# Kernel optimization log

Hardware: AMD Instinct MI355X
Metric: run time of the kernel (lower is better)

## Reference

```python
import jax, jax.numpy as jnp
import numpy as np

N_E, N_R, E = 100000, 1000, 1000000
E_HID, R_HID = 128, 128
NEG_SLOPE = 0.01


def _seg_softmax(logits, seg, num_segments):
    # torch_geometric.utils.softmax: per-segment max-subtracted softmax, +1e-16 in denom
    m = jax.ops.segment_max(logits, seg, num_segments=num_segments)
    m = jnp.where(jnp.isfinite(m), m, 0.0)  # empty segments
    z = jnp.exp(logits - m[seg])
    s = jax.ops.segment_sum(z, seg, num_segments=num_segments)
    return z / (s[seg] + 1e-16)


def setup_inputs() -> dict:
    key = jax.random.key(0)
    ks = jax.random.split(key, 10)
    s_e = 1.0 / np.sqrt(E_HID)
    s_r = 1.0 / np.sqrt(R_HID)
    s_2r = 1.0 / np.sqrt(2 * R_HID)
    return {
        "x_e": jax.random.normal(ks[0], (N_E, E_HID), jnp.float32),
        "x_r": jax.random.normal(ks[1], (N_R, R_HID), jnp.float32),
        "edge_index": jax.random.randint(ks[2], (2, E), 0, N_E, jnp.int32),
        "rel": jax.random.randint(ks[3], (E,), 0, N_R, jnp.int32),
        "rel_all": jax.random.randint(ks[4], (N_R,), 0, N_R, jnp.int32),
        "w_ah": jax.random.uniform(ks[5], (E_HID,), jnp.float32, -s_e, s_e),
        "w_at": jax.random.uniform(ks[6], (E_HID,), jnp.float32, -s_e, s_e),
        "w_ar": jax.random.uniform(ks[7], (R_HID,), jnp.float32, -s_r, s_r),
        "W_r1": jax.random.uniform(ks[8], (R_HID, 2 * R_HID), jnp.float32, -s_r, s_r),
        "b_r1": jnp.zeros((2 * R_HID,), jnp.float32),
        "W_r2": jax.random.uniform(ks[9], (2 * R_HID, R_HID), jnp.float32, -s_2r, s_2r),
        "b_r2": jnp.zeros((R_HID,), jnp.float32),
        "W_r": jax.random.uniform(jax.random.fold_in(key, 99), (2 * R_HID, 2 * R_HID), jnp.float32, -s_2r, s_2r),
        "b_r": jnp.zeros((2 * R_HID,), jnp.float32),
    }


def reference(x_e, x_r, edge_index, rel, rel_all, w_ah, w_at, w_ar,
              W_r1, b_r1, W_r2, b_r2, W_r, b_r):
    h, t = edge_index[0], edge_index[1]
    n_e = x_e.shape[0]

    # per-node/per-rel attention scores, gathered per edge
    e_h = (x_e @ w_ah)[h]          # [E]
    e_t = (x_e @ w_at)[t]          # [E]
    e_r = (x_r @ w_ar)[rel]        # [E]

    alpha_h = _seg_softmax(jax.nn.leaky_relu(e_h + e_r, NEG_SLOPE), h, n_e)
    alpha_t = _seg_softmax(jax.nn.leaky_relu(e_t + e_r, NEG_SLOPE), t, n_e)

    # relation transform (no activation in original)
    x_r2 = (x_r @ W_r1 + b_r1) @ W_r2 + b_r2   # [N_r, r_hidden]
    msg = x_r + x_r2                            # [N_r, r_hidden]

    # sparse.mm(adj, msg) == weighted scatter-add over edges
    msg_e = msg[rel]                            # [E, r_hidden]
    x_e_h = jax.ops.segment_sum(alpha_h[:, None] * msg_e, h, num_segments=n_e)
    x_e_t = jax.ops.segment_sum(alpha_t[:, None] * msg_e, t, num_segments=n_e)

    x = jnp.concatenate([x_e_h, x_e_t], axis=1)  # [N_e, 2*r_hidden]
    return x @ W_r + b_r
```

## Files before the change

kernel.cpp:

```cpp
#include <hip/hip_runtime.h>
#include <hip/hip_fp16.h>


#define CH1    2048
#define SUPW   4096
#define CAP1   45056
#define CH2    4096
#define CHUNK2 (CAP1 / CH2)
#define CAP2   1024
#define MAXD   64

__global__ __launch_bounds__(256) void k_scores(
    const float* __restrict__ xe, const float* __restrict__ xr,
    const float* __restrict__ wah, const float* __restrict__ wat, const float* __restrict__ war,
    float* __restrict__ eh, float* __restrict__ et, float* __restrict__ er,
    int nE, int nR) {
    int wid = (blockIdx.x * blockDim.x + threadIdx.x) >> 6;
    int lane = threadIdx.x & 63;
    if (wid < nE) {
        float2 x2 = *(const float2*)(xe + (size_t)wid * 128 + lane * 2);
        float2 a2 = *(const float2*)(wah + lane * 2);
        float2 b2 = *(const float2*)(wat + lane * 2);
        float dh = x2.x * a2.x + x2.y * a2.y;
        float dt = x2.x * b2.x + x2.y * b2.y;
        #pragma unroll
        for (int m = 32; m >= 1; m >>= 1) { dh += __shfl_xor(dh, m); dt += __shfl_xor(dt, m); }
        if (lane == 0) { eh[wid] = dh; et[wid] = dt; }
    } else if (wid < nE + nR) {
        int r = wid - nE;
        float2 x2 = *(const float2*)(xr + (size_t)r * 128 + lane * 2);
        float2 c2 = *(const float2*)(war + lane * 2);
        float d = x2.x * c2.x + x2.y * c2.y;
        #pragma unroll
        for (int m = 32; m >= 1; m >>= 1) d += __shfl_xor(d, m);
        if (lane == 0) er[r] = d;
    }
}

__global__ __launch_bounds__(256) void k_rel(
    const float* __restrict__ xr,
    const float* __restrict__ W1, const float* __restrict__ b1,
    const float* __restrict__ W2, const float* __restrict__ b2,
    const float* __restrict__ Wr,
    __half* __restrict__ Mh, __half* __restrict__ Mt) {
    __shared__ float xs[128];
    __shared__ float hs[256];
    __shared__ float ms[128];
    int r = blockIdx.x, j = threadIdx.x;
    if (j < 128) xs[j] = xr[(size_t)r * 128 + j];
    __syncthreads();
    {
        float acc = b1[j];
        #pragma unroll 4
        for (int k = 0; k < 128; ++k) acc += xs[k] * W1[k * 256 + j];
        hs[j] = acc;
    }
    __syncthreads();
    if (j < 128) {
        float acc = b2[j] + xs[j];
        #pragma unroll 4
        for (int k = 0; k < 256; ++k) acc += hs[k] * W2[k * 128 + j];
        ms[j] = acc;
    }
    __syncthreads();
    {
        float ah = 0.f, at_ = 0.f;
        #pragma unroll 4
        for (int i = 0; i < 128; ++i) {
            float m = ms[i];
            ah  += m * Wr[i * 256 + j];
            at_ += m * Wr[(128 + i) * 256 + j];
        }
        Mh[(size_t)r * 256 + j] = __float2half(ah);
        Mt[(size_t)r * 256 + j] = __float2half(at_);
    }
}

__global__ __launch_bounds__(256) void k_hist1(
    const int* __restrict__ ei, int* __restrict__ hist, int E) {
    __shared__ int cnt[64];
    int tid = threadIdx.x;
    if (tid < 64) cnt[tid] = 0;
    __syncthreads();
    int base = blockIdx.x * CH1;
    #pragma unroll
    for (int k = 0; k < CH1 / 256; ++k) {
        int e = base + k * 256 + tid;
        if (e < E) {
            unsigned vh = ((unsigned)ei[e]) << 1;
            unsigned vt = (((unsigned)ei[E + e]) << 1) | 1u;
            atomicAdd(&cnt[vh >> 12], 1);
            atomicAdd(&cnt[vt >> 12], 1);
        }
    }
    __syncthreads();
    if (tid < 64) hist[tid * 512 + blockIdx.x] = cnt[tid];
}

__global__ __launch_bounds__(256) void k_scanp(
    int* __restrict__ hist, int* __restrict__ bcur1,
    int* __restrict__ bcur2, int nbuck, int nblk) {
    __shared__ int wtot[4];
    int bin = blockIdx.x, tid = threadIdx.x, lane = tid & 63, wid = tid >> 6;
    int g = bin * 256 + tid;
    if (g < nbuck) bcur2[g] = 0;
    int j0 = 2 * tid, j1 = 2 * tid + 1;
    int v0 = (j0 < nblk) ? hist[bin * 512 + j0] : 0;
    int v1 = (j1 < nblk) ? hist[bin * 512 + j1] : 0;
    int ts = v0 + v1;
    int incl = ts;
    #pragma unroll
    for (int d = 1; d < 64; d <<= 1) { int u = __shfl_up(incl, d); if (lane >= d) incl += u; }
    if (lane == 63) wtot[wid] = incl;
    __syncthreads();
    int wbase = 0;
    for (int w = 0; w < wid; ++w) wbase += wtot[w];
    int excl = wbase + incl - ts;
    hist[bin * 512 + j0] = excl;
    hist[bin * 512 + j1] = excl + v0;
    if (tid == 255) bcur1[bin] = wbase + incl;
}

__global__ __launch_bounds__(256) void k_part1(
    const int* __restrict__ ei, const int* __restrict__ rel,
    const int* __restrict__ hist, unsigned* __restrict__ part1, int E) {
    __shared__ unsigned stage[CH1 * 2];
    __shared__ int cnt[64], offs_[64], cur[64], gb[64];
    int tid = threadIdx.x;
    if (tid < 64) cnt[tid] = 0;
    __syncthreads();
    int base = blockIdx.x * CH1;
    unsigned wh[CH1 / 256], wt[CH1 / 256];
    bool ve[CH1 / 256];
    #pragma unroll
    for (int k = 0; k < CH1 / 256; ++k) {
        int e = base + k * 256 + tid;
        ve[k] = (e < E);
        unsigned h = 0, t = 0, r = 0;
        if (ve[k]) { h = (unsigned)ei[e]; t = (unsigned)ei[E + e]; r = (unsigned)rel[e]; }
        unsigned vh = h << 1, vt = (t << 1) | 1u;
        wh[k] = ((vh >> 12) << 26) | ((vh & 4095u) << 10) | r;
        wt[k] = ((vt >> 12) << 26) | ((vt & 4095u) << 10) | r;
        if (ve[k]) { atomicAdd(&cnt[wh[k] >> 26], 1); atomicAdd(&cnt[wt[k] >> 26], 1); }
    }
    __syncthreads();
    if (tid < 64) {
        int v = cnt[tid], incl = v;
        #pragma unroll
        for (int d = 1; d < 64; d <<= 1) { int u = __shfl_up(incl, d); if (tid >= d) incl += u; }
        offs_[tid] = incl - v;
        cur[tid] = incl - v;
        gb[tid] = hist[tid * 512 + blockIdx.x];
    }
    __syncthreads();
    #pragma unroll
    for (int k = 0; k < CH1 / 256; ++k) {
        if (ve[k]) {
            int p = atomicAdd(&cur[wh[k] >> 26], 1); stage[p] = wh[k];
            int q = atomicAdd(&cur[wt[k] >> 26], 1); stage[q] = wt[k];
        }
    }
    __syncthreads();
    int total = offs_[63] + cnt[63];
    for (int p = tid; p < total; p += 256) {
        unsigned w = stage[p];
        int bin = w >> 26;
        int dst = gb[bin] + (p - offs_[bin]);
        if (dst < CAP1) part1[(size_t)bin * CAP1 + dst] = w & 0x03FFFFFFu;
    }
}

__global__ __launch_bounds__(256) void k_part2(
    const int* __restrict__ bcur1, const unsigned* __restrict__ part1,
    int* __restrict__ bcur2, unsigned short* __restrict__ part2) {
    int s = blockIdx.x / CHUNK2, c = blockIdx.x % CHUNK2;
    int cnt_s = min(bcur1[s], CAP1);
    int start = c * CH2;
    if (start >= cnt_s) return;
    __shared__ unsigned stage[CH2];
    __shared__ int cnt[64], offs_[64], cur[64], gb[64];
    int tid = threadIdx.x;
    if (tid < 64) cnt[tid] = 0;
    __syncthreads();
    unsigned w_[CH2 / 256];
    bool v_[CH2 / 256];
    #pragma unroll
    for (int k = 0; k < CH2 / 256; ++k) {
        int i = start + k * 256 + tid;
        v_[k] = (i < cnt_s);
        unsigned it = v_[k] ? part1[(size_t)s * CAP1 + i] : 0u;
        unsigned sb = (it >> 16) & 63u;
        unsigned entry = (((it >> 10) & 63u) << 10) | (it & 1023u);
        w_[k] = (sb << 16) | entry;
        if (v_[k]) atomicAdd(&cnt[sb], 1);
    }
    __syncthreads();
    if (tid < 64) {
        int v = cnt[tid], incl = v;
        #pragma unroll
        for (int d = 1; d < 64; d <<= 1) { int u = __shfl_up(incl, d); if (tid >= d) incl += u; }
        offs_[tid] = incl - v;
        cur[tid] = incl - v;
        gb[tid] = atomicAdd(&bcur2[s * 64 + tid], v);
    }
    __syncthreads();
    #pragma unroll
    for (int k = 0; k < CH2 / 256; ++k)
        if (v_[k]) { int p = atomicAdd(&cur[w_[k] >> 16], 1); stage[p] = w_[k]; }
    __syncthreads();
    int total = offs_[63] + cnt[63];
    for (int p = tid; p < total; p += 256) {
        unsigned w = stage[p];
        int sb = w >> 16;
        int dst = gb[sb] + (p - offs_[sb]);
        if (dst < CAP2) part2[((size_t)s * 64 + sb) * CAP2 + dst] = (unsigned short)w;
    }
}

__global__ __launch_bounds__(256) void k_group_out6(
    const int* __restrict__ bcur2, const unsigned short* __restrict__ part2,
    const float* __restrict__ eh, const float* __restrict__ et, const float* __restrict__ er,
    const __half* __restrict__ Mh, const __half* __restrict__ Mt,
    const float* __restrict__ br, float* __restrict__ out, int nE, int nR) {
    __shared__ unsigned short csr[CAP2];
    __shared__ float er_s[1024];
    __shared__ int cnt[64], offs_[64], cur[64];
    int b = blockIdx.x, tid = threadIdx.x;
    int count = min(bcur2[b], CAP2);
    if (tid < 64) cnt[tid] = 0;
    for (int i = tid; i < nR; i += 256) er_s[i] = er[i];
    __syncthreads();
    unsigned short ev[CAP2 / 256];
    bool val[CAP2 / 256];
    #pragma unroll
    for (int k = 0; k < CAP2 / 256; ++k) {
        int i = tid + k * 256;
        val[k] = (i < count);
        ev[k] = val[k] ? part2[(size_t)b * CAP2 + i] : (unsigned short)0;
        if (val[k]) atomicAdd(&cnt[ev[k] >> 10], 1);
    }
    __syncthreads();
    if (tid < 64) {
        int v = cnt[tid], incl = v;
        #pragma unroll
        for (int d = 1; d < 64; d <<= 1) { int u = __shfl_up(incl, d); if (tid >= d) incl += u; }
        offs_[tid] = incl - v;
        cur[tid] = incl - v;
    }
    __syncthreads();
    #pragma unroll
    for (int k = 0; k < CAP2 / 256; ++k) {
        if (val[k]) {
            int p = atomicAdd(&cur[ev[k] >> 10], 1);
            csr[p] = (unsigned short)(ev[k] & 1023u);
        }
    }
    __syncthreads();
    int lane = tid & 63, wid = tid >> 6;
    int half = lane >> 5, l31 = lane & 31;
    float4 bv = *(const float4*)(br + l31 * 8 + half * 4);
    int nbase = b * 32;
    for (int li = wid; li < 32; li += 4) {
        int n = nbase + li;
        if (n >= nE) break;
        int oH = offs_[2 * li];
        int oT = offs_[2 * li + 1];
        int dH = min(cur[2 * li] - oH, MAXD);
        int dT = min(cur[2 * li + 1] - oT, MAXD);
        float ehn = eh[n], etn = et[n];
        unsigned eHv = 0u, eTv = 0u;
        if (lane < dH) {
            int r = csr[oH + lane];
            float l = ehn + er_s[r]; l = l > 0.f ? l : 0.01f * l;
            eHv = (__float_as_uint(__expf(l)) & 0xFFFFFC00u) | (unsigned)r;
        }
        if (lane < dT) {
            int r = csr[oT + lane];
            float l = etn + er_s[r]; l = l > 0.f ? l : 0.01f * l;
            eTv = (__float_as_uint(__expf(l)) & 0xFFFFFC00u) | (unsigned)r;
        }
        float aH[8] = {0, 0, 0, 0, 0, 0, 0, 0};
        float aT[8] = {0, 0, 0, 0, 0, 0, 0, 0};
        float sH = 0.f, sT = 0.f;
        for (int j = 0; j < dH; j += 2) {
            unsigned c = (unsigned)__shfl((int)eHv, j + half);
            float z = __uint_as_float(c & 0xFFFFFC00u);
            uint4 m = *(const uint4*)(Mh + (((size_t)(c & 0x3FFu)) << 8) + (l31 << 3));
            const __half* hp = (const __half*)&m;
            #pragma unroll
            for (int q = 0; q < 8; ++q)
                aH[q] = fmaf(__half2float(hp[q]), z, aH[q]);
            sH += z;
        }
        for (int j = 0; j < dT; j += 2) {
            unsigned c = (unsigned)__shfl((int)eTv, j + half);
            float z = __uint_as_float(c & 0xFFFFFC00u);
            uint4 m = *(const uint4*)(Mt + (((size_t)(c & 0x3FFu)) << 8) + (l31 << 3));
            const __half* hp = (const __half*)&m;
            #pragma unroll
            for (int q = 0; q < 8; ++q)
                aT[q] = fmaf(__half2float(hp[q]), z, aT[q]);
            sT += z;
        }
        sH += __shfl_xor(sH, 32);
        sT += __shfl_xor(sT, 32);
        float hc[4], tc[4];
        #pragma unroll
        for (int q = 0; q < 4; ++q) {
            float sendH = half ? aH[q] : aH[4 + q];
            float mineH = half ? aH[4 + q] : aH[q];
            hc[q] = mineH + __shfl_xor(sendH, 32);
            float sendT = half ? aT[q] : aT[4 + q];
            float mineT = half ? aT[4 + q] : aT[q];
            tc[q] = mineT + __shfl_xor(sendT, 32);
        }
        float iH = 1.f / (sH + 1e-16f);
        float iT = 1.f / (sT + 1e-16f);
        float4 o;
        o.x = hc[0] * iH + tc[0] * iT + bv.x;
        o.y = hc[1] * iH + tc[1] * iT + bv.y;
        o.z = hc[2] * iH + tc[2] * iT + bv.z;
        o.w = hc[3] * iH + tc[3] * iT + bv.w;
        *(float4*)(out + (size_t)n * 256 + l31 * 8 + half * 4) = o;
    }
}

__global__ __launch_bounds__(256) void k_hist(
    const int* __restrict__ ei, int* __restrict__ deg, int E, int nE) {
    int e = blockIdx.x * blockDim.x + threadIdx.x;
    if (e >= E) return;
    atomicAdd(&deg[ei[e]], 1);
    atomicAdd(&deg[nE + ei[E + e]], 1);
}

__global__ __launch_bounds__(256) void k_scan1(
    const int* __restrict__ deg, int* __restrict__ offs, int* __restrict__ bsum, int N) {
    __shared__ int wtot[4];
    int tid = threadIdx.x, lane = tid & 63, wid = tid >> 6;
    int base = blockIdx.x * 1024 + tid * 4;
    int v[4];
    #pragma unroll
    for (int i = 0; i < 4; ++i) v[i] = (base + i < N) ? deg[base + i] : 0;
    int ts = v[0] + v[1] + v[2] + v[3];
    int incl = ts;
    #pragma unroll
    for (int d = 1; d < 64; d <<= 1) { int u = __shfl_up(incl, d); if (lane >= d) incl += u; }
    if (lane == 63) wtot[wid] = incl;
    __syncthreads();
    int wbase = 0;
    for (int w = 0; w < wid; ++w) wbase += wtot[w];
    int run = wbase + incl - ts;
    #pragma unroll
    for (int i = 0; i < 4; ++i) { if (base + i < N) offs[base + i] = run; run += v[i]; }
    if (tid == 255) bsum[blockIdx.x] = wbase + incl;
}

__global__ __launch_bounds__(256) void k_scan2(int* __restrict__ bsum, int NB) {
    __shared__ int wtot[4];
    int tid = threadIdx.x, lane = tid & 63, wid = tid >> 6;
    int v = (tid < NB) ? bsum[tid] : 0;
    int incl = v;
    #pragma unroll
    for (int d = 1; d < 64; d <<= 1) { int u = __shfl_up(incl, d); if (lane >= d) incl += u; }
    if (lane == 63) wtot[wid] = incl;
    __syncthreads();
    int wbase = 0;
    for (int w = 0; w < wid; ++w) wbase += wtot[w];
    if (tid < NB) bsum[tid] = wbase + incl - v;
}

__global__ __launch_bounds__(256) void k_scan3(
    int* __restrict__ offs, const int* __restrict__ bsum, int* __restrict__ cursor, int N) {
    int i = blockIdx.x * blockDim.x + threadIdx.x;
    if (i >= N) return;
    int v = offs[i] + bsum[i >> 10];
    offs[i] = v;
    cursor[i] = v;
}

__global__ __launch_bounds__(256) void k_scatter_offs(
    const int* __restrict__ ei, const int* __restrict__ rel,
    const float* __restrict__ eh, const float* __restrict__ et, const float* __restrict__ er,
    int* __restrict__ cursor, unsigned* __restrict__ csr, int E, int nE) {
    int e = blockIdx.x * blockDim.x + threadIdx.x;
    if (e >= E) return;
    int h = ei[e], t = ei[E + e], r = rel[e];
    float erv = er[r];
    float lh = eh[h] + erv; lh = lh > 0.f ? lh : 0.01f * lh;
    float lt = et[t] + erv; lt = lt > 0.f ? lt : 0.01f * lt;
    unsigned zh = (__float_as_uint(__expf(lh)) & 0xFFFFFC00u) | (unsigned)r;
    unsigned zt = (__float_as_uint(__expf(lt)) & 0xFFFFFC00u) | (unsigned)r;
    int ph = atomicAdd(&cursor[h], 1);
    csr[ph] = zh;
    int pt = atomicAdd(&cursor[nE + t], 1);
    csr[pt] = zt;
}

__global__ __launch_bounds__(256) void k_out_offs(
    const int* __restrict__ offs, const int* __restrict__ deg, const unsigned* __restrict__ csr,
    const __half* __restrict__ Mh, const __half* __restrict__ Mt, const float* __restrict__ br,
    float* __restrict__ out, int nE) {
    int wid = (blockIdx.x * blockDim.x + threadIdx.x) >> 6;
    int lane = threadIdx.x & 63;
    if (wid >= nE) return;
    int dH = deg[wid], dT = deg[nE + wid];
    size_t offH = (size_t)offs[wid], offT = (size_t)offs[nE + wid];
    float4 accH = {0, 0, 0, 0}, accT = {0, 0, 0, 0};
    float sH = 0.f, sT = 0.f;
    int dM = max(dH, dT);
    for (int b = 0; b < dM; b += 64) {
        int kH = min(64, dH - b);
        int kT = min(64, dT - b);
        unsigned eH = 0, eT = 0;
        if (lane < kH) eH = csr[offH + b + lane];
        if (lane < kT) eT = csr[offT + b + lane];
        int kk = max(kH, kT);
        for (int j = 0; j < kk; ++j) {
            unsigned cH = (unsigned)__shfl((int)eH, j);
            unsigned cT = (unsigned)__shfl((int)eT, j);
            if (j < kH) {
                float z = __uint_as_float(cH & 0xFFFFFC00u);
                int r = (int)(cH & 0x3FFu);
                const __half2* mp = (const __half2*)(Mh + ((size_t)r << 8) + (lane << 2));
                float2 m01 = __half22float2(mp[0]);
                float2 m23 = __half22float2(mp[1]);
                accH.x += z * m01.x; accH.y += z * m01.y;
                accH.z += z * m23.x; accH.w += z * m23.y;
                sH += z;
            }
            if (j < kT) {
                float z = __uint_as_float(cT & 0xFFFFFC00u);
                int r = (int)(cT & 0x3FFu);
                const __half2* mp = (const __half2*)(Mt + ((size_t)r << 8) + (lane << 2));
                float2 m01 = __half22float2(mp[0]);
                float2 m23 = __half22float2(mp[1]);
                accT.x += z * m01.x; accT.y += z * m01.y;
                accT.z += z * m23.x; accT.w += z * m23.y;
                sT += z;
            }
        }
    }
    float iH = 1.f / (sH + 1e-16f);
    float iT = 1.f / (sT + 1e-16f);
    float4 bv = *(const float4*)(br + lane * 4);
    float4 o;
    o.x = accH.x * iH + accT.x * iT + bv.x;
    o.y = accH.y * iH + accT.y * iT + bv.y;
    o.z = accH.z * iH + accT.z * iT + bv.z;
    o.w = accH.w * iH + accT.w * iT + bv.w;
    *(float4*)(out + (size_t)wid * 256 + lane * 4) = o;
}

extern "C" void kernel_launch(void* const* d_in, const int* in_sizes, int n_in,
                              void* d_out, int out_size, void* d_ws, size_t ws_size,
                              hipStream_t stream) {
    const float* xe  = (const float*)d_in[0];
    const float* xr  = (const float*)d_in[1];
    const int*   ei  = (const int*)d_in[2];
    const int*   rel = (const int*)d_in[3];
    const float* wah = (const float*)d_in[5];
    const float* wat = (const float*)d_in[6];
    const float* war = (const float*)d_in[7];
    const float* W1  = (const float*)d_in[8];
    const float* b1  = (const float*)d_in[9];
    const float* W2  = (const float*)d_in[10];
    const float* b2  = (const float*)d_in[11];
    const float* Wr  = (const float*)d_in[12];
    const float* br  = (const float*)d_in[13];
    float* out = (float*)d_out;

    const int nE = in_sizes[0] / 128;
    const int nR = in_sizes[1] / 128;
    const int E  = in_sizes[3];
    const int N  = 2 * nE;
    const int NSUP  = (N + SUPW - 1) / SUPW;
    const int NBUCK = NSUP * 64;
    const int NBLK1 = (E + CH1 - 1) / CH1;

    float* ws = (float*)d_ws;
    size_t o = 0;
    auto alloc = [&](size_t words) { size_t r = o; o += (words + 3) & ~(size_t)3; return r; };
    float* eh     = ws + alloc(nE);
    float* et     = ws + alloc(nE);
    float* er     = ws + alloc(nR);
    __half* Mh    = (__half*)(ws + alloc((size_t)nR * 128));
    __half* Mt    = (__half*)(ws + alloc((size_t)nR * 128));
    size_t common_words = o;

    size_t hist_words  = 64 * 512;
    size_t part1_words = (size_t)NSUP * CAP1;
    size_t part2_words = ((size_t)NBUCK * CAP2 + 1) / 2;
    size_t new_words = hist_words + 64 + NBUCK + part1_words + part2_words;
    bool planNew = (NBLK1 <= 512) && (NSUP <= 64) &&
                   (ws_size >= (common_words + new_words + 64) * 4);

    k_scores<<<(nE + nR + 3) / 4, 256, 0, stream>>>(xe, xr, wah, wat, war, eh, et, er, nE, nR);
    k_rel<<<nR, 256, 0, stream>>>(xr, W1, b1, W2, b2, Wr, Mh, Mt);

    if (planNew) {
        int* hist   = (int*)(ws + alloc(hist_words));
        int* bcur1  = (int*)(ws + alloc(64));
        int* bcur2  = (int*)(ws + alloc(NBUCK));
        unsigned* part1 = (unsigned*)(ws + alloc(part1_words));
        unsigned short* part2 = (unsigned short*)(ws + alloc(part2_words));
        k_hist1<<<NBLK1, 256, 0, stream>>>(ei, hist, E);
        k_scanp<<<64, 256, 0, stream>>>(hist, bcur1, bcur2, NBUCK, NBLK1);
        k_part1<<<NBLK1, 256, 0, stream>>>(ei, rel, hist, part1, E);
        k_part2<<<NSUP * CHUNK2, 256, 0, stream>>>(bcur1, part1, bcur2, part2);
        k_group_out6<<<NBUCK, 256, 0, stream>>>(bcur2, part2, eh, et, er, Mh, Mt, br, out, nE, nR);
    } else {
        int* cursor = (int*)(ws + alloc(N));
        int* deg    = (int*)(ws + alloc(N));
        int* offs   = (int*)(ws + alloc(N));
        int* bsum   = (int*)(ws + alloc(512));
        unsigned* csr = (unsigned*)(ws + alloc(2 * (size_t)E));
        const int NB = (N + 1023) / 1024;
        hipMemsetAsync(deg, 0, (size_t)N * sizeof(int), stream);
        k_hist<<<(E + 255) / 256, 256, 0, stream>>>(ei, deg, E, nE);
        k_scan1<<<NB, 256, 0, stream>>>(deg, offs, bsum, N);
        k_scan2<<<1, 256, 0, stream>>>(bsum, NB);
        k_scan3<<<(N + 255) / 256, 256, 0, stream>>>(offs, bsum, cursor, N);
        k_scatter_offs<<<(E + 255) / 256, 256, 0, stream>>>(ei, rel, eh, et, er, cursor, csr, E, nE);
        k_out_offs<<<(nE + 3) / 4, 256, 0, stream>>>(offs, deg, csr, Mh, Mt, br, out, nE);
    }
}
```

Before: 325.5 us.

## Split second-level buckets to 16 nodes per block and interleave head/tail gathers

Doubles the number of second-level partition buckets per super-bucket (128 instead of 64), halving each bucket's capacity and the number of nodes handled per output block, so twice as many blocks run the gather-and-project stage. The part2 scan is extended to a two-wave prefix over 128 bins. In the output kernel, the head and tail neighbor loops are merged into one loop so the two independent gathers can overlap, and the per-lane base pointers are hoisted. This trades more blocks, more per-block fixed overhead such as reloading er into shared memory, and more global atomics for better parallelism. It also adds overflow risk from the smaller per-bucket capacity.

```diff
diff --git a/kernel.cpp b/kernel.cpp
--- a/kernel.cpp
+++ b/kernel.cpp
@@ -7,7 +7,8 @@
 #define CAP1   45056
 #define CH2    4096
 #define CHUNK2 (CAP1 / CH2)
-#define CAP2   1024
+#define NBPS   128
+#define CAP2   512
 #define MAXD   64
 
 __global__ __launch_bounds__(256) void k_scores(
@@ -102,8 +103,7 @@
     int* __restrict__ bcur2, int nbuck, int nblk) {
     __shared__ int wtot[4];
     int bin = blockIdx.x, tid = threadIdx.x, lane = tid & 63, wid = tid >> 6;
-    int g = bin * 256 + tid;
-    if (g < nbuck) bcur2[g] = 0;
+    for (int g = bin * 256 + tid; g < nbuck; g += 64 * 256) bcur2[g] = 0;
     int j0 = 2 * tid, j1 = 2 * tid + 1;
     int v0 = (j0 < nblk) ? hist[bin * 512 + j0] : 0;
     int v1 = (j1 < nblk) ? hist[bin * 512 + j1] : 0;
@@ -178,9 +178,10 @@
     int start = c * CH2;
     if (start >= cnt_s) return;
     __shared__ unsigned stage[CH2];
-    __shared__ int cnt[64], offs_[64], cur[64], gb[64];
+    __shared__ int cnt[NBPS], offs_[NBPS], cur[NBPS], gb[NBPS];
+    __shared__ int wt2[2];
     int tid = threadIdx.x;
-    if (tid < 64) cnt[tid] = 0;
+    if (tid < NBPS) cnt[tid] = 0;
     __syncthreads();
     unsigned w_[CH2 / 256];
     bool v_[CH2 / 256];
@@ -189,45 +190,53 @@
         int i = start + k * 256 + tid;
         v_[k] = (i < cnt_s);
         unsigned it = v_[k] ? part1[(size_t)s * CAP1 + i] : 0u;
-        unsigned sb = (it >> 16) & 63u;
-        unsigned entry = (((it >> 10) & 63u) << 10) | (it & 1023u);
+        unsigned sb = ((it >> 10) & 4095u) >> 5;
+        unsigned entry = (((it >> 10) & 31u) << 10) | (it & 1023u);
         w_[k] = (sb << 16) | entry;
         if (v_[k]) atomicAdd(&cnt[sb], 1);
     }
     __syncthreads();
-    if (tid < 64) {
-        int v = cnt[tid], incl = v;
+    int v128 = 0, incl128 = 0;
+    if (tid < NBPS) {
+        v128 = cnt[tid]; incl128 = v128;
+        int lane = tid & 63;
         #pragma unroll
-        for (int d = 1; d < 64; d <<= 1) { int u = __shfl_up(incl, d); if (tid >= d) incl += u; }
-        offs_[tid] = incl - v;
-        cur[tid] = incl - v;
-        gb[tid] = atomicAdd(&bcur2[s * 64 + tid], v);
+        for (int d = 1; d < 64; d <<= 1) { int u = __shfl_up(incl128, d); if (lane >= d) incl128 += u; }
+        if (lane == 63) wt2[tid >> 6] = incl128;
+    }
+    __syncthreads();
+    if (tid < NBPS) {
+        int base2 = (tid >= 64) ? wt2[0] : 0;
+        int excl = base2 + incl128 - v128;
+        offs_[tid] = excl;
+        cur[tid] = excl;
+        gb[tid] = atomicAdd(&bcur2[s * NBPS + tid], v128);
     }
     __syncthreads();
     #pragma unroll
     for (int k = 0; k < CH2 / 256; ++k)
         if (v_[k]) { int p = atomicAdd(&cur[w_[k] >> 16], 1); stage[p] = w_[k]; }
     __syncthreads();
-    int total = offs_[63] + cnt[63];
+    int total = offs_[NBPS - 1] + cnt[NBPS - 1];
     for (int p = tid; p < total; p += 256) {
         unsigned w = stage[p];
         int sb = w >> 16;
         int dst = gb[sb] + (p - offs_[sb]);
-        if (dst < CAP2) part2[((size_t)s * 64 + sb) * CAP2 + dst] = (unsigned short)w;
-    }
-}
-
-__global__ __launch_bounds__(256) void k_group_out6(
+        if (dst < CAP2) part2[((size_t)s * NBPS + sb) * CAP2 + dst] = (unsigned short)w;
+    }
+}
+
+__global__ __launch_bounds__(256) void k_group_out7(
     const int* __restrict__ bcur2, const unsigned short* __restrict__ part2,
     const float* __restrict__ eh, const float* __restrict__ et, const float* __restrict__ er,
     const __half* __restrict__ Mh, const __half* __restrict__ Mt,
     const float* __restrict__ br, float* __restrict__ out, int nE, int nR) {
     __shared__ unsigned short csr[CAP2];
     __shared__ float er_s[1024];
-    __shared__ int cnt[64], offs_[64], cur[64];
+    __shared__ int cnt[32], offs_[32], cur[32];
     int b = blockIdx.x, tid = threadIdx.x;
     int count = min(bcur2[b], CAP2);
-    if (tid < 64) cnt[tid] = 0;
+    if (tid < 32) cnt[tid] = 0;
     for (int i = tid; i < nR; i += 256) er_s[i] = er[i];
     __syncthreads();
     unsigned short ev[CAP2 / 256];
@@ -240,10 +249,10 @@
         if (val[k]) atomicAdd(&cnt[ev[k] >> 10], 1);
     }
     __syncthreads();
-    if (tid < 64) {
+    if (tid < 32) {
         int v = cnt[tid], incl = v;
         #pragma unroll
-        for (int d = 1; d < 64; d <<= 1) { int u = __shfl_up(incl, d); if (tid >= d) incl += u; }
+        for (int d = 1; d < 32; d <<= 1) { int u = __shfl_up(incl, d); if (tid >= d) incl += u; }
         offs_[tid] = incl - v;
         cur[tid] = incl - v;
     }
@@ -258,9 +267,11 @@
     __syncthreads();
     int lane = tid & 63, wid = tid >> 6;
     int half = lane >> 5, l31 = lane & 31;
+    const __half* MhB = Mh + (l31 << 3);
+    const __half* MtB = Mt + (l31 << 3);
     float4 bv = *(const float4*)(br + l31 * 8 + half * 4);
-    int nbase = b * 32;
-    for (int li = wid; li < 32; li += 4) {
+    int nbase = b * 16;
+    for (int li = wid; li < 16; li += 4) {
         int n = nbase + li;
         if (n >= nE) break;
         int oH = offs_[2 * li];
@@ -282,25 +293,28 @@
         float aH[8] = {0, 0, 0, 0, 0, 0, 0, 0};
         float aT[8] = {0, 0, 0, 0, 0, 0, 0, 0};
         float sH = 0.f, sT = 0.f;
-        for (int j = 0; j < dH; j += 2) {
-            unsigned c = (unsigned)__shfl((int)eHv, j + half);
-            float z = __uint_as_float(c & 0xFFFFFC00u);
-            uint4 m = *(const uint4*)(Mh + (((size_t)(c & 0x3FFu)) << 8) + (l31 << 3));
-            const __half* hp = (const __half*)&m;
-            #pragma unroll
-            for (int q = 0; q < 8; ++q)
-                aH[q] = fmaf(__half2float(hp[q]), z, aH[q]);
-            sH += z;
-        }
-        for (int j = 0; j < dT; j += 2) {
-            unsigned c = (unsigned)__shfl((int)eTv, j + half);
-            float z = __uint_as_float(c & 0xFFFFFC00u);
-            uint4 m = *(const uint4*)(Mt + (((size_t)(c & 0x3FFu)) << 8) + (l31 << 3));
-            const __half* hp = (const __half*)&m;
-            #pragma unroll
-            for (int q = 0; q < 8; ++q)
-                aT[q] = fmaf(__half2float(hp[q]), z, aT[q]);
-            sT += z;
+        int kk = max(dH, dT);
+        for (int j = 0; j < kk; j += 2) {
+            if (j < dH) {
+                unsigned c = (unsigned)__shfl((int)eHv, j + half);
+                float z = __uint_as_float(c & 0xFFFFFC00u);
+                uint4 m = *(const uint4*)(MhB + (((size_t)(c & 0x3FFu)) << 8));
+                const __half* hp = (const __half*)&m;
+                #pragma unroll
+                for (int q = 0; q < 8; ++q)
+                    aH[q] = fmaf(__half2float(hp[q]), z, aH[q]);
+                sH += z;
+            }
+            if (j < dT) {
+                unsigned c = (unsigned)__shfl((int)eTv, j + half);
+                float z = __uint_as_float(c & 0xFFFFFC00u);
+                uint4 m = *(const uint4*)(MtB + (((size_t)(c & 0x3FFu)) << 8));
+                const __half* hp = (const __half*)&m;
+                #pragma unroll
+                for (int q = 0; q < 8; ++q)
+                    aT[q] = fmaf(__half2float(hp[q]), z, aT[q]);
+                sT += z;
+            }
         }
         sH += __shfl_xor(sH, 32);
         sT += __shfl_xor(sT, 32);
@@ -474,7 +488,7 @@
     const int E  = in_sizes[3];
     const int N  = 2 * nE;
     const int NSUP  = (N + SUPW - 1) / SUPW;
-    const int NBUCK = NSUP * 64;
+    const int NBUCK = NSUP * NBPS;
     const int NBLK1 = (E + CH1 - 1) / CH1;
 
     float* ws = (float*)d_ws;
@@ -507,7 +521,7 @@
         k_scanp<<<64, 256, 0, stream>>>(hist, bcur1, bcur2, NBUCK, NBLK1);
         k_part1<<<NBLK1, 256, 0, stream>>>(ei, rel, hist, part1, E);
         k_part2<<<NSUP * CHUNK2, 256, 0, stream>>>(bcur1, part1, bcur2, part2);
-        k_group_out6<<<NBUCK, 256, 0, stream>>>(bcur2, part2, eh, et, er, Mh, Mt, br, out, nE, nR);
+        k_group_out7<<<NBUCK, 256, 0, stream>>>(bcur2, part2, eh, et, er, Mh, Mt, br, out, nE, nR);
     } else {
         int* cursor = (int*)(ws + alloc(N));
         int* deg    = (int*)(ws + alloc(N));
```

Measured after the change: 327.3 us. About the same (+0.5%).
